# Kernel tuning notes

Hardware: AMD Instinct MI355X
Metric: run time of the kernel (lower is better)

## Reference

```python
import jax, jax.numpy as jnp
import numpy as np


def _cofactor_antieq(M):
    """ith output = M[...,i,0] * (-1)**i * det(M with row i and col 0 deleted).

    M: (..., n, n) -> (..., n). Vectorized form of the original per-row
    jnp.delete + stack + det construction.
    """
    n = M.shape[-1]
    # rows[i] = all row indices except i, shape (n, n-1)
    rows = np.stack([np.delete(np.arange(n), i) for i in range(n)])
    Msub = M[..., 1:]                 # delete first column: (..., n, n-1)
    sub = Msub[..., rows, :]          # delete row i per output: (..., n, n-1, n-1)
    signs = jnp.asarray((-1.0) ** np.arange(n), dtype=M.dtype)
    return M[..., 0] * signs * jnp.linalg.det(sub)


def setup_inputs() -> dict:
    key = jax.random.key(0)
    ks = jax.random.split(key, 6)
    B, NSPIN, NPS, D, NION, DIM = 4096, 2, 16, 256, 8, 3
    eq_inputs = jax.random.normal(ks[0], (B, NSPIN * NPS, D), jnp.float32)
    r_ei = jax.random.normal(ks[1], (B, NSPIN * NPS, NION, DIM), jnp.float32)
    # per-spin linear orbital params (stacked over spin since splits are equal)
    W = jax.random.normal(ks[2], (NSPIN, D, NPS), jnp.float32) / np.sqrt(D)
    b = jax.random.normal(ks[3], (NSPIN, NPS), jnp.float32) * 0.01
    # anisotropic envelope decay matrices A per (spin, ion, orbital), near identity
    env_dim = jax.random.normal(ks[4], (NSPIN, NION, NPS, DIM, DIM), jnp.float32) * 0.1 + jnp.eye(DIM, dtype=jnp.float32)
    # linear combination over ions per (spin, orbital)
    env_ion = jax.random.normal(ks[5], (NSPIN, NION, NPS), jnp.float32) / NION
    return dict(eq_inputs=eq_inputs, r_ei=r_ei, W=W, b=b, env_dim=env_dim, env_ion=env_ion)


def reference(eq_inputs, r_ei, W, b, env_dim, env_ion):
    B = eq_inputs.shape[0]
    nspin, d, nps = W.shape
    nion, dim = r_ei.shape[-2], r_ei.shape[-1]
    # split particles by spin: (B, nspin, nps, ...)
    xs = eq_inputs.reshape(B, nspin, nps, d)
    rs = r_ei.reshape(B, nspin, nps, nion, dim)
    # linear part of orbitals: (B, s, n, o) with n = o = nps (square per spin)
    y = jnp.einsum('bsnd,sdo->bsno', xs, W) + b[:, None, :]
    # anisotropic exponential envelope: exp(-||A (r - R)||), summed over ions
    Ar = jnp.einsum('sioed,bsnid->bsnioe', env_dim, rs)        # (B,s,n,ion,orb,3)
    env = jnp.einsum('bsnio,sio->bsno',
                     jnp.exp(-jnp.linalg.norm(Ar, axis=-1)), env_ion)
    M = y * env                                                 # (B, s, n, n)
    cof = _cofactor_antieq(M)                                   # (B, s, n)
    return cof[..., None]                                       # (B, s, n, 1)
```

## Files before the change

### kernel.cpp

```cpp
#include <hip/hip_runtime.h>
#include <math.h>


__global__ __launch_bounds__(256)
void cof_fused(const float* __restrict__ eq,
               const float* __restrict__ rei,
               const float* __restrict__ Wm,
               const float* __restrict__ bb,
               const float* __restrict__ edim,
               const float* __restrict__ eion,
               float* __restrict__ out)
{
  __shared__ __align__(16) float Gl[8 * 6 * 16];
  __shared__ __align__(16) float Xl[4 * 320];

  const int tid   = threadIdx.x;
  const int lane  = tid & 63;
  const int wv    = tid >> 6;
  const int blk   = blockIdx.x;
  const int sp    = blk >> 10;
  const int bbase = (blk & 1023) * 4;

  if (tid < 128) {
    const int i = tid >> 4, o = tid & 15;
    const float* A = edim + (((size_t)sp * 8 + i) * 16 + o) * 9;
    const float a0=A[0],a1=A[1],a2=A[2],a3=A[3],a4=A[4],a5=A[5],a6=A[6],a7=A[7],a8=A[8];
    float* Gp = Gl + i * 96 + o;
    Gp[0]  = a0*a0 + a3*a3 + a6*a6;
    Gp[16] = a1*a1 + a4*a4 + a7*a7;
    Gp[32] = a2*a2 + a5*a5 + a8*a8;
    Gp[48] = 2.f*(a0*a1 + a3*a4 + a6*a7);
    Gp[64] = 2.f*(a0*a2 + a3*a5 + a6*a8);
    Gp[80] = 2.f*(a1*a2 + a4*a5 + a7*a8);
  }
  __syncthreads();

  const int bidx = bbase + wv;
  const int cch  = lane >> 4;
  const int nb   = (lane >> 2) & 3;
  const int ob   = lane & 3;

  const float* xb = eq + ((size_t)bidx * 32 + sp * 16) * 256;
  const float* wb = Wm + (size_t)sp * 4096;

  float acc[4][4] = {{0.f,0.f,0.f,0.f},{0.f,0.f,0.f,0.f},
                     {0.f,0.f,0.f,0.f},{0.f,0.f,0.f,0.f}};

  #pragma unroll
  for (int q = 0; q < 16; ++q) {
    const int dg = q * 16 + cch * 4;
    float xr[4][4], wr4[4][4];
    #pragma unroll
    for (int r = 0; r < 4; ++r) {
      float4 t = *(const float4*)(xb + (4 * nb + r) * 256 + dg);
      xr[r][0]=t.x; xr[r][1]=t.y; xr[r][2]=t.z; xr[r][3]=t.w;
    }
    #pragma unroll
    for (int j = 0; j < 4; ++j) {
      float4 t = *(const float4*)(wb + (dg + j) * 16 + 4 * ob);
      wr4[j][0]=t.x; wr4[j][1]=t.y; wr4[j][2]=t.z; wr4[j][3]=t.w;
    }
    #pragma unroll
    for (int r = 0; r < 4; ++r)
      #pragma unroll
      for (int j = 0; j < 4; ++j)
        #pragma unroll
        for (int c2 = 0; c2 < 4; ++c2)
          acc[r][c2] = fmaf(xr[r][j], wr4[j][c2], acc[r][c2]);
  }

  #pragma unroll
  for (int r = 0; r < 4; ++r)
    #pragma unroll
    for (int c2 = 0; c2 < 4; ++c2) {
      float v = acc[r][c2];
      v += __shfl_xor(v, 16);
      v += __shfl_xor(v, 32);
      acc[r][c2] = v;
    }

  float* Mw = Xl + wv * 320;
  {
    float4 bv = *(const float4*)(bb + sp * 16 + 4 * ob);
    if (lane < 16) {
      #pragma unroll
      for (int r = 0; r < 4; ++r) {
        float4 v = make_float4(acc[r][0] + bv.x, acc[r][1] + bv.y,
                               acc[r][2] + bv.z, acc[r][3] + bv.w);
        *(float4*)(Mw + (4 * nb + r) * 20 + 4 * ob) = v;
      }
    }
  }

  {
    const int n = lane >> 2;
    const float* rp = rei + ((size_t)bidx * 32 + sp * 16 + n) * 24;
    float rv[24];
    #pragma unroll
    for (int t4 = 0; t4 < 6; ++t4) {
      float4 t = *(const float4*)(rp + t4 * 4);
      rv[t4*4+0]=t.x; rv[t4*4+1]=t.y; rv[t4*4+2]=t.z; rv[t4*4+3]=t.w;
    }
    float4 env = make_float4(0.f, 0.f, 0.f, 0.f);
    #pragma unroll
    for (int i = 0; i < 8; ++i) {
      const float r0 = rv[i*3], r1 = rv[i*3+1], r2 = rv[i*3+2];
      const float rr0 = r0*r0, rr1 = r1*r1, rr2 = r2*r2;
      const float rr3 = r0*r1, rr4 = r0*r2, rr5 = r1*r2;
      const float* Gp = Gl + i * 96 + 4 * ob;
      const float4 q00 = *(const float4*)(Gp);
      const float4 q11 = *(const float4*)(Gp + 16);
      const float4 q22 = *(const float4*)(Gp + 32);
      const float4 q01 = *(const float4*)(Gp + 48);
      const float4 q02 = *(const float4*)(Gp + 64);
      const float4 q12 = *(const float4*)(Gp + 80);
      const float4 io  = *(const float4*)(eion + ((size_t)sp * 8 + i) * 16 + 4 * ob);
#define ENVC(c) { float n2 = q00.c*rr0 + q11.c*rr1 + q22.c*rr2 \
                           + q01.c*rr3 + q02.c*rr4 + q12.c*rr5; \
                  n2 = fmaxf(n2, 0.f); \
                  env.c += __expf(-sqrtf(n2)) * io.c; }
      ENVC(x) ENVC(y) ENVC(z) ENVC(w)
#undef ENVC
    }
    float* mp = Mw + n * 20 + 4 * ob;
    float4 y = *(const float4*)mp;
    *(float4*)mp = make_float4(y.x * env.x, y.y * env.y, y.z * env.z, y.w * env.w);
  }

  {
    const int r  = lane & 15;
    const int gb = lane & 48;
    float a[16];
    #pragma unroll
    for (int c = 0; c < 16; ++c) a[c] = Mw[c * 20 + r];

    float det = 1.0f;
    int sign = 0;
    unsigned retired = 0;
    unsigned pp0 = 0, pp1 = 0;
    int srr = 0;
    float accf = (r == 0) ? 1.0f : 0.0f;
    float acc2 = 0.0f;

    #pragma unroll
    for (int k = 0; k < 16; ++k) {
      const bool act = ((retired >> r) & 1u) == 0u;
      const float av = act ? fabsf(a[k]) : 0.0f;
      unsigned pk = (__float_as_uint(av) & 0xFFFFFFF0u) | (unsigned)r;
      #pragma unroll
      for (int m = 1; m <= 8; m <<= 1) {
        unsigned o2 = __shfl_xor(pk, m);
        pk = (pk > o2) ? pk : o2;
      }
      const int p = (int)(pk & 15u);
      if (k < 8) pp0 |= (unsigned)p << (4 * k);
      else       pp1 |= (unsigned)p << (4 * (k - 8));
      float pv = __shfl(a[k], gb | p);
      if (fabsf(pv) < 1e-30f) pv = (pv < 0.0f) ? -1e-30f : 1e-30f;
      det *= pv;
      retired |= (1u << p);
      sign ^= (int)(__popc((~retired) & ((1u << p) - 1u)) & 1u);
      if (r == p) srr = k;
      const bool upd = act && (r != p);
      float m2 = 0.0f;
      if (upd) { m2 = a[k] / pv; a[k] = m2; }
      #pragma unroll
      for (int c = k + 1; c < 16; ++c) {
        float bcv = __shfl(a[c], gb | p);
        if (upd) a[c] = fmaf(-m2, bcv, a[c]);
      }
      float zk = __shfl(accf, gb | p);
      if (r == p) acc2 = zk;
      if (upd) accf = fmaf(-m2, zk, accf);
    }
    if (sign) det = -det;

    float myx = 0.0f;
    #pragma unroll
    for (int j = 15; j >= 0; --j) {
      float t = acc2 / a[j];
      const int pj = (int)(((j >= 8) ? (pp1 >> (4 * (j - 8)))
                                     : (pp0 >> (4 * j))) & 15u);
      float xj = __shfl(t, gb | pj);
      if (srr < j) acc2 = fmaf(-a[j], xj, acc2);
      if (r == j) myx = xj;
    }

    const float mi0 = Mw[r * 20];
    const float cof = mi0 * det * myx;
    if (lane < 16)
      out[((size_t)bidx * 2 + sp) * 16 + r] = cof;
  }
}

extern "C" void kernel_launch(void* const* d_in, const int* in_sizes, int n_in,
                              void* d_out, int out_size, void* d_ws, size_t ws_size,
                              hipStream_t stream) {
  (void)in_sizes; (void)n_in; (void)out_size; (void)d_ws; (void)ws_size;
  const float* eq   = (const float*)d_in[0];
  const float* rei  = (const float*)d_in[1];
  const float* Wm   = (const float*)d_in[2];
  const float* bb   = (const float*)d_in[3];
  const float* edim = (const float*)d_in[4];
  const float* eion = (const float*)d_in[5];
  float* out = (float*)d_out;
  hipLaunchKernelGGL(cof_fused, dim3(2048), dim3(256), 0, stream,
                     eq, rei, Wm, bb, edim, eion, out);
}
```

Measured before the change: 232.9 us.

## Split fused kernel into matrix-build and LU-cofactor kernels via workspace

Splits the single fused kernel into two. The first builds the 16x16 orbital-envelope matrices and writes them to global workspace. The second runs the wavefront-level pivoted LU and cofactor solve in 64-thread blocks, four matrices per wavefront. The goal is to separate the register-heavy LU phase from the GEMM/envelope phase so each kernel gets better occupancy. The cost is an extra launch and an 8 MB round trip through global memory.

```diff
diff --git a/kernel.cpp b/kernel.cpp
--- a/kernel.cpp
+++ b/kernel.cpp
@@ -3,13 +3,13 @@
 
 
 __global__ __launch_bounds__(256)
-void cof_fused(const float* __restrict__ eq,
-               const float* __restrict__ rei,
-               const float* __restrict__ Wm,
-               const float* __restrict__ bb,
-               const float* __restrict__ edim,
-               const float* __restrict__ eion,
-               float* __restrict__ out)
+void cof_matrix(const float* __restrict__ eq,
+                const float* __restrict__ rei,
+                const float* __restrict__ Wm,
+                const float* __restrict__ bb,
+                const float* __restrict__ edim,
+                const float* __restrict__ eion,
+                float* __restrict__ ws)
 {
   __shared__ __align__(16) float Gl[8 * 6 * 16];
   __shared__ __align__(16) float Xl[4 * 320];
@@ -122,81 +122,89 @@
       ENVC(x) ENVC(y) ENVC(z) ENVC(w)
 #undef ENVC
     }
-    float* mp = Mw + n * 20 + 4 * ob;
+    const float* mp = Mw + n * 20 + 4 * ob;
     float4 y = *(const float4*)mp;
-    *(float4*)mp = make_float4(y.x * env.x, y.y * env.y, y.z * env.z, y.w * env.w);
-  }
-
-  {
-    const int r  = lane & 15;
-    const int gb = lane & 48;
-    float a[16];
-    #pragma unroll
-    for (int c = 0; c < 16; ++c) a[c] = Mw[c * 20 + r];
-
-    float det = 1.0f;
-    int sign = 0;
-    unsigned retired = 0;
-    unsigned pp0 = 0, pp1 = 0;
-    int srr = 0;
-    float accf = (r == 0) ? 1.0f : 0.0f;
-    float acc2 = 0.0f;
-
-    #pragma unroll
-    for (int k = 0; k < 16; ++k) {
-      const bool act = ((retired >> r) & 1u) == 0u;
-      const float av = act ? fabsf(a[k]) : 0.0f;
-      unsigned pk = (__float_as_uint(av) & 0xFFFFFFF0u) | (unsigned)r;
-      #pragma unroll
-      for (int m = 1; m <= 8; m <<= 1) {
-        unsigned o2 = __shfl_xor(pk, m);
-        pk = (pk > o2) ? pk : o2;
-      }
-      const int p = (int)(pk & 15u);
-      if (k < 8) pp0 |= (unsigned)p << (4 * k);
-      else       pp1 |= (unsigned)p << (4 * (k - 8));
-      float pv = __shfl(a[k], gb | p);
-      if (fabsf(pv) < 1e-30f) pv = (pv < 0.0f) ? -1e-30f : 1e-30f;
-      det *= pv;
-      retired |= (1u << p);
-      sign ^= (int)(__popc((~retired) & ((1u << p) - 1u)) & 1u);
-      if (r == p) srr = k;
-      const bool upd = act && (r != p);
-      float m2 = 0.0f;
-      if (upd) { m2 = a[k] / pv; a[k] = m2; }
-      #pragma unroll
-      for (int c = k + 1; c < 16; ++c) {
-        float bcv = __shfl(a[c], gb | p);
-        if (upd) a[c] = fmaf(-m2, bcv, a[c]);
-      }
-      float zk = __shfl(accf, gb | p);
-      if (r == p) acc2 = zk;
-      if (upd) accf = fmaf(-m2, zk, accf);
-    }
-    if (sign) det = -det;
-
-    float myx = 0.0f;
-    #pragma unroll
-    for (int j = 15; j >= 0; --j) {
-      float t = acc2 / a[j];
-      const int pj = (int)(((j >= 8) ? (pp1 >> (4 * (j - 8)))
-                                     : (pp0 >> (4 * j))) & 15u);
-      float xj = __shfl(t, gb | pj);
-      if (srr < j) acc2 = fmaf(-a[j], xj, acc2);
-      if (r == j) myx = xj;
-    }
-
-    const float mi0 = Mw[r * 20];
-    const float cof = mi0 * det * myx;
-    if (lane < 16)
-      out[((size_t)bidx * 2 + sp) * 16 + r] = cof;
-  }
+    const size_t pair = (size_t)bidx * 2 + sp;
+    *(float4*)(ws + pair * 256 + n * 16 + 4 * ob) =
+        make_float4(y.x * env.x, y.y * env.y, y.z * env.z, y.w * env.w);
+  }
+}
+
+__global__ __launch_bounds__(64)
+void cof_lu(const float* __restrict__ ws,
+            float* __restrict__ out)
+{
+  const int lane = threadIdx.x;
+  const int g  = lane >> 4;
+  const int r  = lane & 15;
+  const int gb = lane & 48;
+  const size_t pair = (size_t)blockIdx.x * 4 + g;
+  const float* mg = ws + pair * 256;
+
+  float a[16];
+  #pragma unroll
+  for (int c = 0; c < 16; ++c) a[c] = mg[c * 16 + r];
+
+  float det = 1.0f;
+  int sign = 0;
+  unsigned retired = 0;
+  unsigned pp0 = 0, pp1 = 0;
+  int srr = 0;
+  float accf = (r == 0) ? 1.0f : 0.0f;
+  float acc2 = 0.0f;
+
+  #pragma unroll
+  for (int k = 0; k < 16; ++k) {
+    const bool act = ((retired >> r) & 1u) == 0u;
+    const float av = act ? fabsf(a[k]) : 0.0f;
+    unsigned pk = (__float_as_uint(av) & 0xFFFFFFF0u) | (unsigned)r;
+    #pragma unroll
+    for (int m = 1; m <= 8; m <<= 1) {
+      unsigned o2 = __shfl_xor(pk, m);
+      pk = (pk > o2) ? pk : o2;
+    }
+    const int p = (int)(pk & 15u);
+    if (k < 8) pp0 |= (unsigned)p << (4 * k);
+    else       pp1 |= (unsigned)p << (4 * (k - 8));
+    float pv = __shfl(a[k], gb | p);
+    if (fabsf(pv) < 1e-30f) pv = (pv < 0.0f) ? -1e-30f : 1e-30f;
+    det *= pv;
+    retired |= (1u << p);
+    sign ^= (int)(__popc((~retired) & ((1u << p) - 1u)) & 1u);
+    if (r == p) srr = k;
+    const bool upd = act && (r != p);
+    float m2 = 0.0f;
+    if (upd) { m2 = a[k] / pv; a[k] = m2; }
+    #pragma unroll
+    for (int c = k + 1; c < 16; ++c) {
+      float bcv = __shfl(a[c], gb | p);
+      if (upd) a[c] = fmaf(-m2, bcv, a[c]);
+    }
+    float zk = __shfl(accf, gb | p);
+    if (r == p) acc2 = zk;
+    if (upd) accf = fmaf(-m2, zk, accf);
+  }
+  if (sign) det = -det;
+
+  float myx = 0.0f;
+  #pragma unroll
+  for (int j = 15; j >= 0; --j) {
+    float t = acc2 / a[j];
+    const int pj = (int)(((j >= 8) ? (pp1 >> (4 * (j - 8)))
+                                   : (pp0 >> (4 * j))) & 15u);
+    float xj = __shfl(t, gb | pj);
+    if (srr < j) acc2 = fmaf(-a[j], xj, acc2);
+    if (r == j) myx = xj;
+  }
+
+  const float mi0 = mg[r * 16];
+  out[pair * 16 + r] = mi0 * det * myx;
 }
 
 extern "C" void kernel_launch(void* const* d_in, const int* in_sizes, int n_in,
                               void* d_out, int out_size, void* d_ws, size_t ws_size,
                               hipStream_t stream) {
-  (void)in_sizes; (void)n_in; (void)out_size; (void)d_ws; (void)ws_size;
+  (void)in_sizes; (void)n_in; (void)out_size; (void)ws_size;
   const float* eq   = (const float*)d_in[0];
   const float* rei  = (const float*)d_in[1];
   const float* Wm   = (const float*)d_in[2];
@@ -204,6 +212,8 @@
   const float* edim = (const float*)d_in[4];
   const float* eion = (const float*)d_in[5];
   float* out = (float*)d_out;
-  hipLaunchKernelGGL(cof_fused, dim3(2048), dim3(256), 0, stream,
-                     eq, rei, Wm, bb, edim, eion, out);
+  float* ws  = (float*)d_ws;
+  hipLaunchKernelGGL(cof_matrix, dim3(2048), dim3(256), 0, stream,
+                     eq, rei, Wm, bb, edim, eion, ws);
+  hipLaunchKernelGGL(cof_lu, dim3(2048), dim3(64), 0, stream, ws, out);
 }
```

New measurement: 236.9 us. About the same (+1.7%).
